# Optimization experiments

Measured on AMD Instinct MI355X. Metric: run time of the kernel, lower is better.

The kernel has to match this reference:

```python
import jax, jax.numpy as jnp
import numpy as np

B, C, H, W = 4, 64, 256, 256
HEADS, WS, DIL = 4, 3, 2
HD = C // HEADS            # 16
HID = 256
EPS = 1e-5
PAD = DIL * (WS // 2)      # 2
K = WS * WS                # 9 neighbors


def setup_inputs() -> dict:
    key = jax.random.key(0)
    ks = jax.random.split(key, 8)
    s = 0.05
    return {
        "x": jax.random.normal(ks[0], (B, C, H, W), jnp.float32),
        "gamma1": jnp.ones((C,), jnp.float32),
        "beta1": jnp.zeros((C,), jnp.float32),
        "gamma2": jnp.ones((C,), jnp.float32),
        "beta2": jnp.zeros((C,), jnp.float32),
        "w_qkv": jax.random.normal(ks[1], (3 * C, C), jnp.float32) * s,
        "b_qkv": jax.random.normal(ks[2], (3 * C,), jnp.float32) * s,
        "w_out": jax.random.normal(ks[3], (C, C), jnp.float32) * s,
        "b_out": jax.random.normal(ks[4], (C,), jnp.float32) * s,
        "w1": jax.random.normal(ks[5], (HID, C), jnp.float32) * s,
        "b1": jax.random.normal(ks[6], (HID,), jnp.float32) * s,
        "w2": jax.random.normal(ks[7], (C, HID), jnp.float32) * s,
        "b2": jnp.zeros((C,), jnp.float32),
    }


def _ln(x, g, b):
    # LayerNorm over channel dim of [B,C,H,W]
    mu = jnp.mean(x, axis=1, keepdims=True)
    var = jnp.mean(jnp.square(x - mu), axis=1, keepdims=True)
    xn = (x - mu) * jax.lax.rsqrt(var + EPS)
    return xn * g[None, :, None, None] + b[None, :, None, None]


def _conv1x1(x, w, b):
    # x: [B,Cin,H,W], w: [Cout,Cin]
    y = jnp.einsum('bchw,oc->bohw', x, w)
    return y + b[None, :, None, None]


def _gather_neighbors(t):
    # t: [B,heads,H,W,hd] -> [B,heads,H,W,K,hd] with zero boundary padding
    tp = jnp.pad(t, ((0, 0), (0, 0), (PAD, PAD), (PAD, PAD), (0, 0)))
    views = [tp[:, :, i * DIL:i * DIL + H, j * DIL:j * DIL + W, :]
             for i in range(WS) for j in range(WS)]
    return jnp.stack(views, axis=4)


def _attn(x, w_qkv, b_qkv, w_out, b_out):
    qkv = _conv1x1(x, w_qkv, b_qkv)                       # [B,3C,H,W]
    qkv = qkv.reshape(B, 3, HEADS, HD, H, W)
    qkv = jnp.transpose(qkv, (1, 0, 2, 4, 5, 3))          # [3,B,heads,H,W,hd]
    q, k, v = qkv[0], qkv[1], qkv[2]
    k_nb = _gather_neighbors(k)                           # [B,heads,H,W,K,hd]
    v_nb = _gather_neighbors(v)
    scale = HD ** -0.5
    scores = jnp.einsum('bnhwd,bnhwkd->bnhwk', q * scale, k_nb)
    attn = jax.nn.softmax(scores, axis=-1)
    out = jnp.einsum('bnhwk,bnhwkd->bnhwd', attn, v_nb)   # [B,heads,H,W,hd]
    out = jnp.transpose(out, (0, 1, 4, 2, 3)).reshape(B, C, H, W)
    return _conv1x1(out, w_out, b_out)


def reference(x, gamma1, beta1, gamma2, beta2, w_qkv, b_qkv, w_out, b_out, w1, b1, w2, b2):
    # pre-norm: x = x + attn(norm1(x)); x = x + mlp(norm2(x))
    x = x + _attn(_ln(x, gamma1, beta1), w_qkv, b_qkv, w_out, b_out)
    h = jax.nn.gelu(_conv1x1(_ln(x, gamma2, beta2), w1, b1), approximate=False)
    m = jax.nn.gelu(_conv1x1(h, w2, b2), approximate=False)
    return x + m
```

## Files before the change

### kernel.cpp

```cpp
#include <hip/hip_runtime.h>
#include <math.h>

#define HW    65536
#define EPSLN 1e-5f

typedef unsigned short ushort_t;
typedef __attribute__((ext_vector_type(8))) short bf16x8;
typedef __attribute__((ext_vector_type(4))) short bf16x4;
typedef __attribute__((ext_vector_type(4))) float f32x4;

#define QKV_USHORTS (4*192*65536)
#define WQ_H 0
#define WQ_L 12288
#define W1_H 24576
#define W1_L 40960
#define W2_H 57344
#define W2_L 73728
#define WO_H 90112
#define WO_L 94208

__device__ __forceinline__ ushort_t f2bf(float f) {
    unsigned u = __float_as_uint(f);
    return (ushort_t)((u + 0x7FFFu + ((u >> 16) & 1u)) >> 16);
}
__device__ __forceinline__ float bf2f(ushort_t h) {
    return __uint_as_float(((unsigned)h) << 16);
}
__device__ __forceinline__ float gelu_fast(float v) {
    float u  = v * v * v;
    float z2 = 1.5957691216057308f * v + 0.07135481627283788f * u;
    float e  = __expf(z2);
    float th = 1.f - 2.f * __builtin_amdgcn_rcpf(1.f + e);
    return 0.5f * v * (1.f + th);
}

__global__ void k_prep(const float* __restrict__ wq, const float* __restrict__ w1,
                       const float* __restrict__ w2, const float* __restrict__ wo,
                       ushort_t* __restrict__ wb)
{
    int i = blockIdx.x * 256 + threadIdx.x;
    float v; int oh, ol;
    if (i < 12288)      { v = wq[i];          oh = WQ_H + i;          ol = WQ_L + i; }
    else if (i < 28672) { int j = i - 12288;  v = w1[j]; oh = W1_H+j; ol = W1_L+j; }
    else if (i < 45056) { int j = i - 28672;  v = w2[j]; oh = W2_H+j; ol = W2_L+j; }
    else                { int j = i - 45056;  v = wo[j]; oh = WO_H+j; ol = WO_L+j; }
    ushort_t h = f2bf(v);
    wb[oh] = h;
    wb[ol] = f2bf(v - bf2f(h));
}

__global__ __launch_bounds__(256, 4) void k_lnqkv_mfma(
    const float* __restrict__ x,  const float* __restrict__ g1,
    const float* __restrict__ b1, const ushort_t* __restrict__ wb,
    const float* __restrict__ bq, ushort_t* __restrict__ qkv)
{
    __shared__ float sg1[64], sb1[64], sbq[192];
    int tid = threadIdx.x;
    if (tid < 64) { sg1[tid] = g1[tid]; sb1[tid] = b1[tid]; }
    if (tid < 192) sbq[tid] = bq[tid];
    __syncthreads();

    int wave = tid >> 6, lane = tid & 63;
    int g = lane >> 4, q = lane & 15;
    int wgl = blockIdx.x * 4 + wave;
    int px0 = wgl * 64;
    int b   = px0 >> 16;
    int hwb = px0 & 65535;
    const float* xb = x + (size_t)b * 64 * HW;

    bf16x8 bh[4][2];
#pragma unroll
    for (int pg = 0; pg < 4; ++pg) {
        int hw = hwb + pg * 16 + q;
        const float* xp = xb + hw;
        float xv[16];
#pragma unroll
        for (int j = 0; j < 8; ++j) {
            xv[j]     = xp[(g * 8 + j) * HW];
            xv[8 + j] = xp[(32 + g * 8 + j) * HW];
        }
        float s = 0.f;
#pragma unroll
        for (int j = 0; j < 16; ++j) s += xv[j];
        s += __shfl_xor(s, 16); s += __shfl_xor(s, 32);
        float mu = s * 0.015625f;
        float s2 = 0.f;
#pragma unroll
        for (int j = 0; j < 16; ++j) { float d = xv[j] - mu; s2 += d * d; }
        s2 += __shfl_xor(s2, 16); s2 += __shfl_xor(s2, 32);
        float inv = rsqrtf(s2 * 0.015625f + EPSLN);
#pragma unroll
        for (int kt = 0; kt < 2; ++kt)
#pragma unroll
            for (int j = 0; j < 8; ++j) {
                int c = kt * 32 + g * 8 + j;
                float f = (xv[kt * 8 + j] - mu) * inv * sg1[c] + sb1[c];
                bh[pg][kt][j] = (short)f2bf(f);
            }
    }

    const ushort_t* wqh = wb + WQ_H;
    const ushort_t* wql = wb + WQ_L;
    ushort_t* outb = qkv + (size_t)b * 12 * HW * 16;

#pragma unroll 2
    for (int mt = 0; mt < 12; ++mt) {
        bf16x8 ah[2], al[2];
#pragma unroll
        for (int kt = 0; kt < 2; ++kt) {
            ah[kt] = *(const bf16x8*)(wqh + (mt * 16 + q) * 64 + kt * 32 + g * 8);
            al[kt] = *(const bf16x8*)(wql + (mt * 16 + q) * 64 + kt * 32 + g * 8);
        }
        f32x4 bias = *(const f32x4*)(&sbq[mt * 16 + 4 * g]);
#pragma unroll
        for (int pg = 0; pg < 4; ++pg) {
            f32x4 d = bias;
#pragma unroll
            for (int kt = 0; kt < 2; ++kt) {
                d = __builtin_amdgcn_mfma_f32_16x16x32_bf16(ah[kt], bh[pg][kt], d, 0, 0, 0);
                d = __builtin_amdgcn_mfma_f32_16x16x32_bf16(al[kt], bh[pg][kt], d, 0, 0, 0);
            }
            bf16x4 st;
#pragma unroll
            for (int i = 0; i < 4; ++i) st[i] = (short)f2bf(d[i]);
            int hw = hwb + pg * 16 + q;
            *(bf16x4*)(outb + ((size_t)mt * HW + hw) * 16 + 4 * g) = st;
        }
    }
}

__global__ __launch_bounds__(256) void k_attn_mfma(
    const float* __restrict__ x, const ushort_t* __restrict__ qkv,
    const ushort_t* __restrict__ wb, const float* __restrict__ bo,
    float* __restrict__ x1)
{
    __shared__ ushort_t abuf[4][64 * 64];
    __shared__ float sbo[64];
    int tid = threadIdx.x, wave = tid >> 6, lane = tid & 63;
    if (tid < 64) sbo[tid] = bo[tid];
    __syncthreads();

    int px = blockIdx.x * 256 + tid;
    int b = px >> 16, hw = px & 65535;
    int hh = hw >> 8, ww = hw & 255;
    const ushort_t* tb = qkv + (size_t)b * 12 * HW * 16;

    int   nidx[9];
    float nmask[9];
#pragma unroll
    for (int n = 0; n < 9; ++n) {
        int dy = (n / 3) * 2 - 2, dx = (n % 3) * 2 - 2;
        int y = hh + dy, xw = ww + dx;
        int yc = min(max(y, 0), 255), xc = min(max(xw, 0), 255);
        nidx[n]  = yc * 256 + xc;
        nmask[n] = (y == yc && xw == xc) ? 1.f : 0.f;
    }

#pragma unroll 1
    for (int head = 0; head < 4; ++head) {
        const ushort_t* qp = tb + ((size_t)head * HW + hw) * 16;
        bf16x8 q0 = *(const bf16x8*)qp;
        bf16x8 q1 = *(const bf16x8*)(qp + 8);
        float qv[16];
#pragma unroll
        for (int j = 0; j < 8; ++j) {
            qv[j]     = bf2f((ushort_t)q0[j]) * 0.25f;
            qv[8 + j] = bf2f((ushort_t)q1[j]) * 0.25f;
        }
        const ushort_t* kb = tb + (size_t)(4 + head) * HW * 16;
        const ushort_t* vb = tb + (size_t)(8 + head) * HW * 16;

        float sc[9];
#pragma unroll
        for (int n = 0; n < 9; ++n) {
            const ushort_t* kp = kb + (size_t)nidx[n] * 16;
            bf16x8 k0 = *(const bf16x8*)kp;
            bf16x8 k1 = *(const bf16x8*)(kp + 8);
            float s = 0.f;
#pragma unroll
            for (int j = 0; j < 8; ++j) {
                s += qv[j]     * bf2f((ushort_t)k0[j]);
                s += qv[8 + j] * bf2f((ushort_t)k1[j]);
            }
            sc[n] = s * nmask[n];
        }
        float mx = sc[0];
#pragma unroll
        for (int n = 1; n < 9; ++n) mx = fmaxf(mx, sc[n]);

        float ew[9], sum = 0.f;
#pragma unroll
        for (int n = 0; n < 9; ++n) {
            float e = __expf(sc[n] - mx);
            sum += e;
            ew[n] = e * nmask[n];
        }

        float o16[16];
#pragma unroll
        for (int d = 0; d < 16; ++d) o16[d] = 0.f;
#pragma unroll
        for (int n = 0; n < 9; ++n) {
            const ushort_t* vp = vb + (size_t)nidx[n] * 16;
            bf16x8 v0 = *(const bf16x8*)vp;
            bf16x8 v1 = *(const bf16x8*)(vp + 8);
            float a = ew[n];
#pragma unroll
            for (int j = 0; j < 8; ++j) {
                o16[j]     += a * bf2f((ushort_t)v0[j]);
                o16[8 + j] += a * bf2f((ushort_t)v1[j]);
            }
        }
        float isum = __builtin_amdgcn_rcpf(sum);

        bf16x8 w0, w1v;
#pragma unroll
        for (int j = 0; j < 8; ++j) {
            w0[j]  = (short)f2bf(o16[j] * isum);
            w1v[j] = (short)f2bf(o16[8 + j] * isum);
        }
        int c0 = (head * 2)     ^ (lane & 7);
        int c1 = (head * 2 + 1) ^ (lane & 7);
        *(bf16x8*)(&abuf[wave][lane * 64 + c0 * 8]) = w0;
        *(bf16x8*)(&abuf[wave][lane * 64 + c1 * 8]) = w1v;
    }
    __syncthreads();

    int g = lane >> 4, q = lane & 15;
    const ushort_t* woh = wb + WO_H;
    const ushort_t* wol = wb + WO_L;
    int hwwb = (blockIdx.x * 256 + wave * 64) & 65535;

#pragma unroll 1
    for (int pg = 0; pg < 4; ++pg) {
        int r = pg * 16 + q;
        bf16x8 bb[2];
#pragma unroll
        for (int kt = 0; kt < 2; ++kt) {
            int c = (kt * 4 + g) ^ (r & 7);
            bb[kt] = *(const bf16x8*)(&abuf[wave][r * 64 + c * 8]);
        }
        int hwg = hwwb + pg * 16 + q;
#pragma unroll
        for (int mt = 0; mt < 4; ++mt) {
            f32x4 d = *(const f32x4*)(&sbo[mt * 16 + 4 * g]);
#pragma unroll
            for (int kt = 0; kt < 2; ++kt) {
                bf16x8 ah = *(const bf16x8*)(woh + (mt * 16 + q) * 64 + kt * 32 + g * 8);
                bf16x8 al = *(const bf16x8*)(wol + (mt * 16 + q) * 64 + kt * 32 + g * 8);
                d = __builtin_amdgcn_mfma_f32_16x16x32_bf16(ah, bb[kt], d, 0, 0, 0);
                d = __builtin_amdgcn_mfma_f32_16x16x32_bf16(al, bb[kt], d, 0, 0, 0);
            }
#pragma unroll
            for (int i = 0; i < 4; ++i) {
                int o = mt * 16 + 4 * g + i;
                size_t idx = (size_t)(b * 64 + o) * HW + hwg;
                x1[idx] = x[idx] + d[i];
            }
        }
    }
}

__global__ __launch_bounds__(256, 3) void k_mlp_mfma(
    const float* __restrict__ g2, const float* __restrict__ b2,
    const ushort_t* __restrict__ wb,
    const float* __restrict__ bb1, const float* __restrict__ bb2,
    float* __restrict__ io)
{
    __shared__ ushort_t hbh[4][2][2048];
    __shared__ float sg2[64], sb2[64], sbb1[256], sbb2[64];
    int tid = threadIdx.x;
    sbb1[tid] = bb1[tid];
    if (tid < 64) { sg2[tid] = g2[tid]; sb2[tid] = b2[tid]; sbb2[tid] = bb2[tid]; }
    __syncthreads();

    int wave = tid >> 6, lane = tid & 63;
    int g = lane >> 4, q = lane & 15;
    int wgl = blockIdx.x * 4 + wave;
    int px0 = wgl * 64;
    int b   = px0 >> 16;
    int hwb = px0 & 65535;
    float* iob = io + (size_t)b * 64 * HW;

    bf16x8 bh[4][2];
#pragma unroll
    for (int pg = 0; pg < 4; ++pg) {
        int hw = hwb + pg * 16 + q;
        const float* xp = iob + hw;
        float xv[16];
#pragma unroll
        for (int j = 0; j < 8; ++j) {
            xv[j]     = xp[(g * 8 + j) * HW];
            xv[8 + j] = xp[(32 + g * 8 + j) * HW];
        }
        float s = 0.f;
#pragma unroll
        for (int j = 0; j < 16; ++j) s += xv[j];
        s += __shfl_xor(s, 16); s += __shfl_xor(s, 32);
        float mu = s * 0.015625f;
        float s2 = 0.f;
#pragma unroll
        for (int j = 0; j < 16; ++j) { float d = xv[j] - mu; s2 += d * d; }
        s2 += __shfl_xor(s2, 16); s2 += __shfl_xor(s2, 32);
        float inv = rsqrtf(s2 * 0.015625f + EPSLN);
#pragma unroll
        for (int kt = 0; kt < 2; ++kt)
#pragma unroll
            for (int j = 0; j < 8; ++j) {
                int c = kt * 32 + g * 8 + j;
                float f = (xv[kt * 8 + j] - mu) * inv * sg2[c] + sb2[c];
                bh[pg][kt][j] = (short)f2bf(f);
            }
    }

    const ushort_t* w1h = wb + W1_H;  const ushort_t* w1l = wb + W1_L;
    const ushort_t* w2h = wb + W2_H;  const ushort_t* w2l = wb + W2_L;

    f32x4 acc2[4][4];
#pragma unroll
    for (int m2 = 0; m2 < 4; ++m2) {
        f32x4 binit = *(const f32x4*)(&sbb2[m2 * 16 + 4 * g]);
#pragma unroll
        for (int pg = 0; pg < 4; ++pg) acc2[pg][m2] = binit;
    }

#pragma unroll 1
    for (int mtp = 0; mtp < 8; ++mtp) {
        int buf = mtp & 1;
#pragma unroll
        for (int e = 0; e < 2; ++e) {
            int mt = mtp * 2 + e;
            bf16x8 ah[2], al[2];
#pragma unroll
            for (int kt = 0; kt < 2; ++kt) {
                ah[kt] = *(const bf16x8*)(w1h + (mt * 16 + q) * 64 + kt * 32 + g * 8);
                al[kt] = *(const bf16x8*)(w1l + (mt * 16 + q) * 64 + kt * 32 + g * 8);
            }
            f32x4 b1v = *(const f32x4*)(&sbb1[mt * 16 + 4 * g]);
            int chunk = (e * 4 + g) ^ (q & 6);
#pragma unroll
            for (int pg = 0; pg < 4; ++pg) {
                f32x4 d = b1v;
#pragma unroll
                for (int kt = 0; kt < 2; ++kt) {
                    d = __builtin_amdgcn_mfma_f32_16x16x32_bf16(ah[kt], bh[pg][kt], d, 0, 0, 0);
                    d = __builtin_amdgcn_mfma_f32_16x16x32_bf16(al[kt], bh[pg][kt], d, 0, 0, 0);
                }
                bf16x4 vh;
#pragma unroll
                for (int i = 0; i < 4; ++i)
                    vh[i] = (short)f2bf(gelu_fast(d[i]));
                *(bf16x4*)(&hbh[wave][buf][pg * 512 + q * 32 + chunk * 4]) = vh;
            }
        }
        int c0 = (2 * g) ^ (q & 6);
        bf16x8 p2[4];
#pragma unroll
        for (int pg = 0; pg < 4; ++pg)
            p2[pg] = *(const bf16x8*)(&hbh[wave][buf][pg * 512 + q * 32 + c0 * 4]);
#pragma unroll
        for (int m2 = 0; m2 < 4; ++m2) {
            bf16x8 ah2 = *(const bf16x8*)(w2h + (m2 * 16 + q) * 256 + mtp * 32 + g * 8);
            bf16x8 al2 = *(const bf16x8*)(w2l + (m2 * 16 + q) * 256 + mtp * 32 + g * 8);
#pragma unroll
            for (int pg = 0; pg < 4; ++pg) {
                acc2[pg][m2] = __builtin_amdgcn_mfma_f32_16x16x32_bf16(ah2, p2[pg], acc2[pg][m2], 0, 0, 0);
                acc2[pg][m2] = __builtin_amdgcn_mfma_f32_16x16x32_bf16(al2, p2[pg], acc2[pg][m2], 0, 0, 0);
            }
        }
    }

#pragma unroll
    for (int pg = 0; pg < 4; ++pg)
#pragma unroll
        for (int m2 = 0; m2 < 4; ++m2)
#pragma unroll
            for (int i = 0; i < 4; ++i) {
                int o = m2 * 16 + 4 * g + i;
                int hw = hwb + pg * 16 + q;
                float m = gelu_fast(acc2[pg][m2][i]);
                iob[(size_t)o * HW + hw] = iob[(size_t)o * HW + hw] + m;
            }
}

extern "C" void kernel_launch(void* const* d_in, const int* in_sizes, int n_in,
                              void* d_out, int out_size, void* d_ws, size_t ws_size,
                              hipStream_t stream)
{
    const float* x     = (const float*)d_in[0];
    const float* g1    = (const float*)d_in[1];
    const float* b1    = (const float*)d_in[2];
    const float* g2    = (const float*)d_in[3];
    const float* b2    = (const float*)d_in[4];
    const float* w_qkv = (const float*)d_in[5];
    const float* b_qkv = (const float*)d_in[6];
    const float* w_out = (const float*)d_in[7];
    const float* b_out = (const float*)d_in[8];
    const float* w1    = (const float*)d_in[9];
    const float* bb1   = (const float*)d_in[10];
    const float* w2    = (const float*)d_in[11];
    const float* bb2   = (const float*)d_in[12];

    float*    out = (float*)d_out;
    ushort_t* qkv = (ushort_t*)d_ws;
    ushort_t* wb  = (ushort_t*)d_ws + QKV_USHORTS;

    k_prep      <<<192,  256, 0, stream>>>(w_qkv, w1, w2, w_out, wb);
    k_lnqkv_mfma<<<1024, 256, 0, stream>>>(x, g1, b1, wb, b_qkv, qkv);
    k_attn_mfma <<<1024, 256, 0, stream>>>(x, qkv, wb, b_out, out);
    k_mlp_mfma  <<<1024, 256, 0, stream>>>(g2, b2, wb, bb1, bb2, out);
}
```

Before: 338.9 us.

## Switch main kernels to single-wave blocks and restructure out-projection loop

All three main kernels now launch one wavefront (64 threads) per block instead of four, with 4x more blocks. Per-wave shared memory indexing is removed and launch bounds are set to raise the register budget and resident block count per CU. The attention kernel's output projection now preloads all activation fragments and hoists the Wo weight loads per output tile, so weights are loaded once per tile rather than once per pixel group. The trade-off is more blocks to schedule, repeated per-block loading of biases and norm parameters, and higher register pressure from holding all fragments.

```diff
diff --git a/kernel.cpp b/kernel.cpp
--- a/kernel.cpp
+++ b/kernel.cpp
@@ -49,21 +49,21 @@
     wb[ol] = f2bf(v - bf2f(h));
 }
 
-__global__ __launch_bounds__(256, 4) void k_lnqkv_mfma(
+__global__ __launch_bounds__(64, 5) void k_lnqkv_mfma(
     const float* __restrict__ x,  const float* __restrict__ g1,
     const float* __restrict__ b1, const ushort_t* __restrict__ wb,
     const float* __restrict__ bq, ushort_t* __restrict__ qkv)
 {
     __shared__ float sg1[64], sb1[64], sbq[192];
     int tid = threadIdx.x;
-    if (tid < 64) { sg1[tid] = g1[tid]; sb1[tid] = b1[tid]; }
-    if (tid < 192) sbq[tid] = bq[tid];
+    sg1[tid] = g1[tid]; sb1[tid] = b1[tid];
+#pragma unroll
+    for (int i = tid; i < 192; i += 64) sbq[i] = bq[i];
     __syncthreads();
 
-    int wave = tid >> 6, lane = tid & 63;
+    int lane = tid;
     int g = lane >> 4, q = lane & 15;
-    int wgl = blockIdx.x * 4 + wave;
-    int px0 = wgl * 64;
+    int px0 = blockIdx.x * 64;
     int b   = px0 >> 16;
     int hwb = px0 & 65535;
     const float* xb = x + (size_t)b * 64 * HW;
@@ -129,18 +129,18 @@
     }
 }
 
-__global__ __launch_bounds__(256) void k_attn_mfma(
+__global__ __launch_bounds__(64, 4) void k_attn_mfma(
     const float* __restrict__ x, const ushort_t* __restrict__ qkv,
     const ushort_t* __restrict__ wb, const float* __restrict__ bo,
     float* __restrict__ x1)
 {
-    __shared__ ushort_t abuf[4][64 * 64];
+    __shared__ ushort_t abuf[64 * 64];
     __shared__ float sbo[64];
-    int tid = threadIdx.x, wave = tid >> 6, lane = tid & 63;
-    if (tid < 64) sbo[tid] = bo[tid];
+    int lane = threadIdx.x;
+    sbo[lane] = bo[lane];
     __syncthreads();
 
-    int px = blockIdx.x * 256 + tid;
+    int px = blockIdx.x * 64 + lane;
     int b = px >> 16, hw = px & 65535;
     int hh = hw >> 8, ww = hw & 255;
     const ushort_t* tb = qkv + (size_t)b * 12 * HW * 16;
@@ -221,63 +221,73 @@
         }
         int c0 = (head * 2)     ^ (lane & 7);
         int c1 = (head * 2 + 1) ^ (lane & 7);
-        *(bf16x8*)(&abuf[wave][lane * 64 + c0 * 8]) = w0;
-        *(bf16x8*)(&abuf[wave][lane * 64 + c1 * 8]) = w1v;
+        *(bf16x8*)(&abuf[lane * 64 + c0 * 8]) = w0;
+        *(bf16x8*)(&abuf[lane * 64 + c1 * 8]) = w1v;
     }
     __syncthreads();
 
     int g = lane >> 4, q = lane & 15;
     const ushort_t* woh = wb + WO_H;
     const ushort_t* wol = wb + WO_L;
-    int hwwb = (blockIdx.x * 256 + wave * 64) & 65535;
-
-#pragma unroll 1
+    int hwwb = (blockIdx.x * 64) & 65535;
+    const float* xb = x + (size_t)b * 64 * HW;
+    float* x1b = x1 + (size_t)b * 64 * HW;
+
+    bf16x8 bb[4][2];
+#pragma unroll
     for (int pg = 0; pg < 4; ++pg) {
         int r = pg * 16 + q;
-        bf16x8 bb[2];
 #pragma unroll
         for (int kt = 0; kt < 2; ++kt) {
             int c = (kt * 4 + g) ^ (r & 7);
-            bb[kt] = *(const bf16x8*)(&abuf[wave][r * 64 + c * 8]);
-        }
-        int hwg = hwwb + pg * 16 + q;
-#pragma unroll
-        for (int mt = 0; mt < 4; ++mt) {
-            f32x4 d = *(const f32x4*)(&sbo[mt * 16 + 4 * g]);
+            bb[pg][kt] = *(const bf16x8*)(&abuf[r * 64 + c * 8]);
+        }
+    }
+
+#pragma unroll 1
+    for (int mt = 0; mt < 4; ++mt) {
+        bf16x8 ah[2], al[2];
+#pragma unroll
+        for (int kt = 0; kt < 2; ++kt) {
+            ah[kt] = *(const bf16x8*)(woh + (mt * 16 + q) * 64 + kt * 32 + g * 8);
+            al[kt] = *(const bf16x8*)(wol + (mt * 16 + q) * 64 + kt * 32 + g * 8);
+        }
+        f32x4 bias = *(const f32x4*)(&sbo[mt * 16 + 4 * g]);
+#pragma unroll
+        for (int pg = 0; pg < 4; ++pg) {
+            f32x4 d = bias;
 #pragma unroll
             for (int kt = 0; kt < 2; ++kt) {
-                bf16x8 ah = *(const bf16x8*)(woh + (mt * 16 + q) * 64 + kt * 32 + g * 8);
-                bf16x8 al = *(const bf16x8*)(wol + (mt * 16 + q) * 64 + kt * 32 + g * 8);
-                d = __builtin_amdgcn_mfma_f32_16x16x32_bf16(ah, bb[kt], d, 0, 0, 0);
-                d = __builtin_amdgcn_mfma_f32_16x16x32_bf16(al, bb[kt], d, 0, 0, 0);
-            }
+                d = __builtin_amdgcn_mfma_f32_16x16x32_bf16(ah[kt], bb[pg][kt], d, 0, 0, 0);
+                d = __builtin_amdgcn_mfma_f32_16x16x32_bf16(al[kt], bb[pg][kt], d, 0, 0, 0);
+            }
+            int hwg = hwwb + pg * 16 + q;
 #pragma unroll
             for (int i = 0; i < 4; ++i) {
                 int o = mt * 16 + 4 * g + i;
-                size_t idx = (size_t)(b * 64 + o) * HW + hwg;
-                x1[idx] = x[idx] + d[i];
-            }
-        }
-    }
-}
-
-__global__ __launch_bounds__(256, 3) void k_mlp_mfma(
+                x1b[(size_t)o * HW + hwg] = xb[(size_t)o * HW + hwg] + d[i];
+            }
+        }
+    }
+}
+
+__global__ __launch_bounds__(64, 6) void k_mlp_mfma(
     const float* __restrict__ g2, const float* __restrict__ b2,
     const ushort_t* __restrict__ wb,
     const float* __restrict__ bb1, const float* __restrict__ bb2,
     float* __restrict__ io)
 {
-    __shared__ ushort_t hbh[4][2][2048];
+    __shared__ ushort_t hbh[2][2048];
     __shared__ float sg2[64], sb2[64], sbb1[256], sbb2[64];
     int tid = threadIdx.x;
-    sbb1[tid] = bb1[tid];
-    if (tid < 64) { sg2[tid] = g2[tid]; sb2[tid] = b2[tid]; sbb2[tid] = bb2[tid]; }
+    sg2[tid] = g2[tid]; sb2[tid] = b2[tid]; sbb2[tid] = bb2[tid];
+#pragma unroll
+    for (int i = tid; i < 256; i += 64) sbb1[i] = bb1[i];
     __syncthreads();
 
-    int wave = tid >> 6, lane = tid & 63;
+    int lane = tid;
     int g = lane >> 4, q = lane & 15;
-    int wgl = blockIdx.x * 4 + wave;
-    int px0 = wgl * 64;
+    int px0 = blockIdx.x * 64;
     int b   = px0 >> 16;
     int hwb = px0 & 65535;
     float* iob = io + (size_t)b * 64 * HW;
@@ -350,14 +360,14 @@
 #pragma unroll
                 for (int i = 0; i < 4; ++i)
                     vh[i] = (short)f2bf(gelu_fast(d[i]));
-                *(bf16x4*)(&hbh[wave][buf][pg * 512 + q * 32 + chunk * 4]) = vh;
+                *(bf16x4*)(&hbh[buf][pg * 512 + q * 32 + chunk * 4]) = vh;
             }
         }
         int c0 = (2 * g) ^ (q & 6);
         bf16x8 p2[4];
 #pragma unroll
         for (int pg = 0; pg < 4; ++pg)
-            p2[pg] = *(const bf16x8*)(&hbh[wave][buf][pg * 512 + q * 32 + c0 * 4]);
+            p2[pg] = *(const bf16x8*)(&hbh[buf][pg * 512 + q * 32 + c0 * 4]);
 #pragma unroll
         for (int m2 = 0; m2 < 4; ++m2) {
             bf16x8 ah2 = *(const bf16x8*)(w2h + (m2 * 16 + q) * 256 + mtp * 32 + g * 8);
@@ -406,7 +416,7 @@
     ushort_t* wb  = (ushort_t*)d_ws + QKV_USHORTS;
 
     k_prep      <<<192,  256, 0, stream>>>(w_qkv, w1, w2, w_out, wb);
-    k_lnqkv_mfma<<<1024, 256, 0, stream>>>(x, g1, b1, wb, b_qkv, qkv);
-    k_attn_mfma <<<1024, 256, 0, stream>>>(x, qkv, wb, b_out, out);
-    k_mlp_mfma  <<<1024, 256, 0, stream>>>(g2, b2, wb, bb1, bb2, out);
-}
+    k_lnqkv_mfma<<<4096, 64, 0, stream>>>(x, g1, b1, wb, b_qkv, qkv);
+    k_attn_mfma <<<4096, 64, 0, stream>>>(x, qkv, wb, b_out, out);
+    k_mlp_mfma  <<<4096, 64, 0, stream>>>(g2, b2, wb, bb1, bb2, out);
+}
```

After: 292.3 us. 13.8% less time.
